# Kernel tuning notes

Hardware: AMD Instinct MI355X
Metric: run time of the kernel (lower is better)

The kernel has to match this reference:

```python
import jax, jax.numpy as jnp
import numpy as np

NUM_TASKS = 1024
N_FEATURES = 256
HIDDEN = 64
BATCH = 8192


def setup_inputs() -> dict:
    key = jax.random.key(0)
    k1, k2, k3, k4, k5 = jax.random.split(key, 5)
    x = jax.random.normal(k1, (BATCH, N_FEATURES), dtype=jnp.float32)
    task_ids = jax.random.randint(k2, (BATCH,), 0, NUM_TASKS, dtype=jnp.int32)
    # embedding tables, stored flat like nn.Embedding.weight
    l1_emb = jax.random.normal(k3, (NUM_TASKS, HIDDEN * N_FEATURES), dtype=jnp.float32) * 0.02
    l2_emb = jax.random.normal(k4, (NUM_TASKS, HIDDEN * HIDDEN), dtype=jnp.float32) * 0.02
    l3_emb = jax.random.normal(k5, (NUM_TASKS, HIDDEN), dtype=jnp.float32) * 0.02
    return {"x": x, "task_ids": task_ids, "l1_emb": l1_emb, "l2_emb": l2_emb, "l3_emb": l3_emb}


def reference(x, task_ids, l1_emb, l2_emb, l3_emb):
    # gather per-sample weight matrices (torch: emb.weight[task_ids].view(...))
    l1 = l1_emb[task_ids].reshape(-1, N_FEATURES, HIDDEN)   # [B, F, H]
    l2 = l2_emb[task_ids].reshape(-1, HIDDEN, HIDDEN)        # [B, H, H]
    l3 = l3_emb[task_ids]                                    # [B, H]
    gelu = lambda v: jax.nn.gelu(v, approximate=False)       # torch nn.GELU default = exact erf
    h1 = gelu(jnp.einsum('bf,bfh->bh', x, l1))               # [B, H]
    h2 = gelu(jnp.einsum('bh,bhk->bk', h1, l2))              # [B, H]
    out = jnp.einsum('bh,bh->b', h2, l3)[:, None]            # [B, 1] (matches squeeze(-1) of [B,1,1])
    return jax.nn.sigmoid(out)
```

## Files before the change

### kernel.cpp

```cpp
#include <hip/hip_runtime.h>
#include <math.h>

#define BATCH 8192
#define NTASK 1024
#define NF 256
#define NH 64
#define MAXBLK 2816


__global__ __launch_bounds__(1024) void prep_kernel(const int* __restrict__ task_ids,
                                                    int* __restrict__ order,
                                                    int* __restrict__ desc,
                                                    int* __restrict__ nblk) {
    __shared__ int cnt[NTASK];
    __shared__ int tmp[NTASK];
    __shared__ int off[NTASK];
    const int tid = threadIdx.x;

    cnt[tid] = 0;
    __syncthreads();
    #pragma unroll
    for (int k = 0; k < 8; ++k)
        atomicAdd(&cnt[task_ids[tid + k * 1024]], 1);
    __syncthreads();

    const int c = cnt[tid];
    tmp[tid] = c;
    __syncthreads();
    for (int d = 1; d < NTASK; d <<= 1) {
        int t_ = (tid >= d) ? tmp[tid - d] : 0;
        __syncthreads();
        tmp[tid] += t_;
        __syncthreads();
    }
    off[tid] = tmp[tid] - c;
    cnt[tid] = off[tid];
    __syncthreads();

    #pragma unroll
    for (int k = 0; k < 8; ++k) {
        int i = tid + k * 1024;
        int t = task_ids[i];
        int pos = atomicAdd(&cnt[t], 1);
        order[pos] = i;
    }

    const int nb = (c + 3) >> 2;
    __syncthreads();
    tmp[tid] = nb;
    __syncthreads();
    for (int d = 1; d < NTASK; d <<= 1) {
        int t_ = (tid >= d) ? tmp[tid - d] : 0;
        __syncthreads();
        tmp[tid] += t_;
        __syncthreads();
    }
    int bstart = tmp[tid] - nb;
    for (int k = 0; k < nb; ++k) {
        int start = off[tid] + 4 * k;
        int S = min(4, c - 4 * k);
        desc[bstart + k] = (tid << 15) | (start << 2) | (S - 1);
    }
    if (tid == NTASK - 1) nblk[0] = tmp[tid];
}

__device__ __forceinline__ float gelu_exact(float s) {
    return 0.5f * s * (1.f + erff(s * 0.70710678118654752440f));
}
__device__ __forceinline__ float4 gelu4(float4 v) {
    return make_float4(gelu_exact(v.x), gelu_exact(v.y), gelu_exact(v.z), gelu_exact(v.w));
}
__device__ __forceinline__ float4 fma4(float s, float4 w, float4 a) {
    a.x = fmaf(s, w.x, a.x); a.y = fmaf(s, w.y, a.y);
    a.z = fmaf(s, w.z, a.z); a.w = fmaf(s, w.w, a.w);
    return a;
}
__device__ __forceinline__ float4 xor_reduce4(float4 v, int m) {
    v.x += __shfl_xor(v.x, m); v.y += __shfl_xor(v.y, m);
    v.z += __shfl_xor(v.z, m); v.w += __shfl_xor(v.w, m);
    return v;
}

__global__ __launch_bounds__(256) void mlp_quad(
    const float* __restrict__ x,
    const int*   __restrict__ order,
    const int*   __restrict__ desc,
    const int*   __restrict__ nblk,
    const float* __restrict__ l1_emb,
    const float* __restrict__ l2_emb,
    const float* __restrict__ l3_emb,
    float*       __restrict__ out)
{
    const int nb = nblk[0];
    const int P  = blockIdx.x;
    if (P >= nb) return;
    const int qc = nb >> 3, r = nb & 7;
    const int xcd = P & 7, j = P >> 3;
    const int b = (xcd < r ? xcd * (qc + 1) : r * (qc + 1) + (xcd - r) * qc) + j;

    const int d  = desc[b];
    const int S  = (d & 3) + 1;
    const int st = (d >> 2) & 8191;
    const int t  = d >> 15;

    const int tid  = threadIdx.x;
    const int lane = tid & 63;
    const int w    = tid >> 6;
    const int cq   = lane & 15;
    const int grp  = lane >> 4;

    __shared__ float  xs[4][NF];
    __shared__ float4 red[4][4][16];
    __shared__ float4 h1s[4][16];
    __shared__ int    sidx[4];

    if (tid < 4) sidx[tid] = order[st + (tid < S ? tid : 0)];
    __syncthreads();

    {
        const float4* x4 = (const float4*)x;
        int s = tid >> 6, qq = tid & 63;
        ((float4*)xs)[s * 64 + qq] = x4[(size_t)sidx[s] * 64 + qq];
    }
    __syncthreads();

    const float4* W1 = (const float4*)(l1_emb + (size_t)t * (NF * NH));
    float4 a0 = make_float4(0.f,0.f,0.f,0.f), a1 = a0, a2 = a0, a3 = a0;
    const int fbase = w * 64 + grp * 16;
    #pragma unroll
    for (int jj = 0; jj < 16; ++jj) {
        const int f = fbase + jj;
        float4 wv = W1[f * 16 + cq];
        a0 = fma4(xs[0][f], wv, a0);
        a1 = fma4(xs[1][f], wv, a1);
        a2 = fma4(xs[2][f], wv, a2);
        a3 = fma4(xs[3][f], wv, a3);
    }
    a0 = xor_reduce4(xor_reduce4(a0, 16), 32);
    a1 = xor_reduce4(xor_reduce4(a1, 16), 32);
    a2 = xor_reduce4(xor_reduce4(a2, 16), 32);
    a3 = xor_reduce4(xor_reduce4(a3, 16), 32);
    if (lane < 16) {
        red[w][0][lane] = a0; red[w][1][lane] = a1;
        red[w][2][lane] = a2; red[w][3][lane] = a3;
    }
    __syncthreads();
    if (tid < 64) {
        int s = tid >> 4, qq = tid & 15;
        float4 A = red[0][s][qq], B = red[1][s][qq], C = red[2][s][qq], D = red[3][s][qq];
        h1s[s][qq] = gelu4(make_float4(A.x+B.x+C.x+D.x, A.y+B.y+C.y+D.y,
                                       A.z+B.z+C.z+D.z, A.w+B.w+C.w+D.w));
    }
    __syncthreads();

    const float4* W2 = (const float4*)(l2_emb + (size_t)t * (NH * NH));
    const float4  hv = h1s[w][grp];
    float4 acc = make_float4(0.f,0.f,0.f,0.f);
    {
        float4 wv0 = W2[(grp * 4 + 0) * 16 + cq];
        float4 wv1 = W2[(grp * 4 + 1) * 16 + cq];
        float4 wv2 = W2[(grp * 4 + 2) * 16 + cq];
        float4 wv3 = W2[(grp * 4 + 3) * 16 + cq];
        acc = fma4(hv.x, wv0, acc);
        acc = fma4(hv.y, wv1, acc);
        acc = fma4(hv.z, wv2, acc);
        acc = fma4(hv.w, wv3, acc);
    }
    acc = xor_reduce4(xor_reduce4(acc, 16), 32);
    float4 g = gelu4(acc);

    const float4* L3 = (const float4*)(l3_emb + (size_t)t * NH);
    float4 w3 = L3[cq];
    float dot = g.x * w3.x + g.y * w3.y + g.z * w3.z + g.w * w3.w;
    #pragma unroll
    for (int m = 1; m < 16; m <<= 1) dot += __shfl_xor(dot, m);
    if (lane == 0 && w < S)
        out[sidx[w]] = 1.f / (1.f + expf(-dot));
}

extern "C" void kernel_launch(void* const* d_in, const int* in_sizes, int n_in,
                              void* d_out, int out_size, void* d_ws, size_t ws_size,
                              hipStream_t stream) {
    const float* x        = (const float*)d_in[0];
    const int*   task_ids = (const int*)  d_in[1];
    const float* l1_emb   = (const float*)d_in[2];
    const float* l2_emb   = (const float*)d_in[3];
    const float* l3_emb   = (const float*)d_in[4];
    float*       out      = (float*)d_out;

    int* ws    = (int*)d_ws;
    int* order = ws;
    int* desc  = ws + BATCH;
    int* nblk  = ws + BATCH + MAXBLK;

    prep_kernel<<<1, 1024, 0, stream>>>(task_ids, order, desc, nblk);
    mlp_quad   <<<MAXBLK, 256, 0, stream>>>(x, order, desc, nblk,
                                            l1_emb, l2_emb, l3_emb, out);
}
```

Measured before the change: 32.47 us.

## Use wavefront shuffle scans in prep and drop extra barriers in MLP kernel

The prep kernel replaces two 1024-thread shared-memory Hillis-Steele scans, each with about 20 barriers, by a single packed wave-level shuffle scan plus a small cross-wave scan. It also caches task ids in registers instead of reloading them. The MLP kernel loads each sample index per wave directly, which removes a barrier and the sidx array. It also has every wave compute the GELU of its own layer-1 reduction redundantly, removing the h1s staging and another barrier. The packed scan assumes counts and block totals fit in 12 bits each.

Measured after the change: 28.70 us. -11.6%, faster.

```diff
diff --git a/kernel.cpp b/kernel.cpp
--- a/kernel.cpp
+++ b/kernel.cpp
@@ -13,55 +13,62 @@
                                                     int* __restrict__ desc,
                                                     int* __restrict__ nblk) {
     __shared__ int cnt[NTASK];
-    __shared__ int tmp[NTASK];
-    __shared__ int off[NTASK];
-    const int tid = threadIdx.x;
+    __shared__ int wsum[16];
+    const int tid  = threadIdx.x;
+    const int lane = tid & 63;
+    const int wv   = tid >> 6;
 
     cnt[tid] = 0;
     __syncthreads();
+
+    int myids[8];
     #pragma unroll
-    for (int k = 0; k < 8; ++k)
-        atomicAdd(&cnt[task_ids[tid + k * 1024]], 1);
+    for (int k = 0; k < 8; ++k) myids[k] = task_ids[tid + k * 1024];
+    #pragma unroll
+    for (int k = 0; k < 8; ++k) atomicAdd(&cnt[myids[k]], 1);
     __syncthreads();
 
-    const int c = cnt[tid];
-    tmp[tid] = c;
+    const int c  = cnt[tid];
+    const int nb = (c + 3) >> 2;
+    const int packed = (c << 12) | nb;
+
+    int v = packed;
+    #pragma unroll
+    for (int d = 1; d < 64; d <<= 1) {
+        int u = __shfl_up(v, d);
+        if (lane >= d) v += u;
+    }
+    if (lane == 63) wsum[wv] = v;
     __syncthreads();
-    for (int d = 1; d < NTASK; d <<= 1) {
-        int t_ = (tid >= d) ? tmp[tid - d] : 0;
-        __syncthreads();
-        tmp[tid] += t_;
-        __syncthreads();
+    if (wv == 0 && lane < 16) {
+        int s = wsum[lane];
+        #pragma unroll
+        for (int d = 1; d < 16; d <<= 1) {
+            int u = __shfl_up(s, d);
+            if (lane >= d) s += u;
+        }
+        wsum[lane] = s;
     }
-    off[tid] = tmp[tid] - c;
-    cnt[tid] = off[tid];
+    __syncthreads();
+
+    const int incl = ((wv > 0) ? wsum[wv - 1] : 0) + v;
+    const int excl = incl - packed;
+    const int offC   = excl >> 12;
+    const int bstart = excl & 0xFFF;
+    if (tid == NTASK - 1) nblk[0] = incl & 0xFFF;
+    cnt[tid] = offC;
     __syncthreads();
 
     #pragma unroll
     for (int k = 0; k < 8; ++k) {
         int i = tid + k * 1024;
-        int t = task_ids[i];
-        int pos = atomicAdd(&cnt[t], 1);
+        int pos = atomicAdd(&cnt[myids[k]], 1);
         order[pos] = i;
     }
-
-    const int nb = (c + 3) >> 2;
-    __syncthreads();
-    tmp[tid] = nb;
-    __syncthreads();
-    for (int d = 1; d < NTASK; d <<= 1) {
-        int t_ = (tid >= d) ? tmp[tid - d] : 0;
-        __syncthreads();
-        tmp[tid] += t_;
-        __syncthreads();
+    for (int k = 0; k < nb; ++k) {
+        int S = min(4, c - 4 * k);
+        desc[bstart + k] = (tid << 15) | ((offC + 4 * k) << 2) | (S - 1);
     }
-    int bstart = tmp[tid] - nb;
-    for (int k = 0; k < nb; ++k) {
-        int start = off[tid] + 4 * k;
-        int S = min(4, c - 4 * k);
-        desc[bstart + k] = (tid << 15) | (start << 2) | (S - 1);
-    }
-    if (tid == NTASK - 1) nblk[0] = tmp[tid];
 }
 
 __device__ __forceinline__ float gelu_exact(float s) {
@@ -111,16 +118,12 @@
 
     __shared__ float  xs[4][NF];
     __shared__ float4 red[4][4][16];
-    __shared__ float4 h1s[4][16];
-    __shared__ int    sidx[4];
 
-    if (tid < 4) sidx[tid] = order[st + (tid < S ? tid : 0)];
-    __syncthreads();
+    const int myi = order[st + min(w, S - 1)];
 
     {
         const float4* x4 = (const float4*)x;
-        int s = tid >> 6, qq = tid & 63;
-        ((float4*)xs)[s * 64 + qq] = x4[(size_t)sidx[s] * 64 + qq];
+        ((float4*)xs)[w * 64 + lane] = x4[(size_t)myi * 64 + lane];
     }
     __syncthreads();
 
@@ -145,27 +148,18 @@
         red[w][2][lane] = a2; red[w][3][lane] = a3;
     }
     __syncthreads();
-    if (tid < 64) {
-        int s = tid >> 4, qq = tid & 15;
-        float4 A = red[0][s][qq], B = red[1][s][qq], C = red[2][s][qq], D = red[3][s][qq];
-        h1s[s][qq] = gelu4(make_float4(A.x+B.x+C.x+D.x, A.y+B.y+C.y+D.y,
-                                       A.z+B.z+C.z+D.z, A.w+B.w+C.w+D.w));
-    }
-    __syncthreads();
+
+    float4 A = red[0][w][grp], B = red[1][w][grp];
+    float4 C = red[2][w][grp], D = red[3][w][grp];
+    const float4 hv = gelu4(make_float4(A.x+B.x+C.x+D.x, A.y+B.y+C.y+D.y,
+                                        A.z+B.z+C.z+D.z, A.w+B.w+C.w+D.w));
 
     const float4* W2 = (const float4*)(l2_emb + (size_t)t * (NH * NH));
-    const float4  hv = h1s[w][grp];
     float4 acc = make_float4(0.f,0.f,0.f,0.f);
-    {
-        float4 wv0 = W2[(grp * 4 + 0) * 16 + cq];
-        float4 wv1 = W2[(grp * 4 + 1) * 16 + cq];
-        float4 wv2 = W2[(grp * 4 + 2) * 16 + cq];
-        float4 wv3 = W2[(grp * 4 + 3) * 16 + cq];
-        acc = fma4(hv.x, wv0, acc);
-        acc = fma4(hv.y, wv1, acc);
-        acc = fma4(hv.z, wv2, acc);
-        acc = fma4(hv.w, wv3, acc);
-    }
+    acc = fma4(hv.x, W2[(grp * 4 + 0) * 16 + cq], acc);
+    acc = fma4(hv.y, W2[(grp * 4 + 1) * 16 + cq], acc);
+    acc = fma4(hv.z, W2[(grp * 4 + 2) * 16 + cq], acc);
+    acc = fma4(hv.w, W2[(grp * 4 + 3) * 16 + cq], acc);
     acc = xor_reduce4(xor_reduce4(acc, 16), 32);
     float4 g = gelu4(acc);
 
@@ -175,7 +169,7 @@
     #pragma unroll
     for (int m = 1; m < 16; m <<= 1) dot += __shfl_xor(dot, m);
     if (lane == 0 && w < S)
-        out[sidx[w]] = 1.f / (1.f + expf(-dot));
+        out[myi] = 1.f / (1.f + expf(-dot));
 }
 
 extern "C" void kernel_launch(void* const* d_in, const int* in_sizes, int n_in,
```
